# Kernel optimization log

Hardware: AMD Instinct MI355X
Metric: run time of the kernel (lower is better)

Reference implementation:

```python
import jax, jax.numpy as jnp
import numpy as np

# Production-scale dims: CSA layer on a 64x64, 512-channel decoder feature map
B, C, H, W = 8, 512, 64, 64
HOLE = 32  # centered square hole side -> M = 1024 masked points, N = 3072 context points
EPS = 1e-8


def _mask_and_indices():
    m = np.zeros((H, W), np.float32)
    r0, c0 = (H - HOLE) // 2, (W - HOLE) // 2
    m[r0:r0 + HOLE, c0:c0 + HOLE] = 1.0
    flat = m.reshape(-1)
    mask_idx = np.nonzero(flat > 0.5)[0].astype(np.int32)      # masked (hole) flat positions, raster order
    nonmask_idx = np.nonzero(flat <= 0.5)[0].astype(np.int32)  # known (context) flat positions
    return m, nonmask_idx, mask_idx


def setup_inputs() -> dict:
    key = jax.random.key(0)
    x = jax.random.normal(key, (B, C, H, W), dtype=jnp.float32)
    m, nm, mi = _mask_and_indices()
    return {
        "input": x,
        "mask": jnp.asarray(m),
        "nonmask_point_idx": jnp.asarray(nm),
        "mask_point_idx": jnp.asarray(mi),
    }


def _csa(x, nonmask_point_idx, mask_point_idx):
    """Coherent Semantic Attention with 1x1 patches (shift_sz=1, stride=1).

    For each masked location (raster order): find the most-similar context
    patch by cosine similarity, then coherently blend it with the previously
    generated patch, weighted by their respective similarities.
    """
    b, c, h, w = x.shape
    feats = x.reshape(b, c, h * w)                      # [B,C,HW] 1x1 patches
    ctx = feats[:, :, nonmask_point_idx]                # [B,C,N] known/context patches
    msk = feats[:, :, mask_point_idx]                   # [B,C,M] masked patches
    ctx_n = ctx / (jnp.linalg.norm(ctx, axis=1, keepdims=True) + EPS)
    msk_n = msk / (jnp.linalg.norm(msk, axis=1, keepdims=True) + EPS)

    # cross cosine similarity: dominant compute (B*M*N*C)
    cos = jnp.einsum('bcm,bcn->bmn', msk_n, ctx_n)      # [B,M,N]
    maxc = cos.max(axis=-1)                             # [B,M] best context similarity
    amax = cos.argmax(axis=-1)                          # [B,M]
    # gather the best-matching (unnormalized) context patch per masked point
    best = jnp.take_along_axis(ctx.transpose(0, 2, 1), amax[..., None], axis=1)  # [B,M,C]

    xs = (msk_n.transpose(2, 0, 1),   # [M,B,C] normalized masked patches
          best.transpose(1, 0, 2),    # [M,B,C] best context patches
          maxc.T)                     # [M,B]

    def step(prev, inp):
        mn, bst, mx = inp
        prev_n = prev / (jnp.linalg.norm(prev, axis=-1, keepdims=True) + EPS)
        d_ad = jnp.maximum(jnp.sum(mn * prev_n, axis=-1), 0.0)   # [B] coherence with previous generated patch
        cur = (d_ad[:, None] * prev + mx[:, None] * bst) / (d_ad + mx + EPS)[:, None]
        return cur, cur

    # prev initialized to zeros -> d_ad = 0 for the first masked patch (pure context copy)
    _, gen = jax.lax.scan(step, jnp.zeros((b, c), x.dtype), xs)   # [M,B,C]

    out = feats.at[:, :, mask_point_idx].set(gen.transpose(1, 2, 0))
    return out.reshape(b, c, h, w)


def reference(input, mask, nonmask_point_idx, mask_point_idx):
    return _csa(input, nonmask_point_idx, mask_point_idx)
```

## Files before the change

kernel.cpp:

```cpp
#include <hip/hip_runtime.h>
#include <hip/hip_bf16.h>

#define B_   8
#define C_   512
#define HW_  4096
#define M_   1024
#define N_   3072
#define EPS_ 1e-8f

typedef __attribute__((ext_vector_type(4))) float f32x4;
typedef __attribute__((ext_vector_type(8))) short short8;

__global__ void k_norms(const float* __restrict__ x, float* __restrict__ inv_all) {
    int blk = blockIdx.x;
    int b = blk >> 5;
    int chunk = blk & 31;
    int hw = chunk * 128 + threadIdx.x;
    const float* xb = x + (size_t)b * C_ * HW_;
    float acc = 0.f;
#pragma unroll 8
    for (int c = 0; c < C_; ++c) {
        float v = xb[(size_t)c * HW_ + hw];
        acc = fmaf(v, v, acc);
    }
    inv_all[b * HW_ + hw] = 1.0f / (sqrtf(acc) + EPS_);
}

__global__ __launch_bounds__(256) void k_pack(const float* __restrict__ x,
    const int* __restrict__ nm_idx, const int* __restrict__ m_idx,
    const float* __restrict__ inv_all,
    unsigned int* __restrict__ Apk, unsigned int* __restrict__ Bpk,
    float* __restrict__ invM, float* __restrict__ invC)
{
    __shared__ float T[32][513];
    __shared__ int ps[32];
    int blk = blockIdx.x;
    int t = threadIdx.x;
    int isA = blk < 256;
    int b, grp;
    const int* idxarr;
    if (isA) { b = blk >> 5; grp = blk & 31; idxarr = m_idx; }
    else     { int r = blk - 256; b = r / 96; grp = r % 96; idxarr = nm_idx; }
    const float* xb = x + (size_t)b * C_ * HW_;
    if (t < 32) {
        int p = idxarr[grp * 32 + t];
        ps[t] = p;
        float iv = inv_all[b * HW_ + p];
        if (isA) invM[b * 1024 + grp * 32 + t] = iv;
        else     invC[b * 3072 + grp * 32 + t] = iv;
    }
    __syncthreads();
#pragma unroll 4
    for (int rep = 0; rep < 64; ++rep) {
        int idx = rep * 256 + t;
        int c = idx >> 5, i = idx & 31;
        T[i][c] = xb[(size_t)c * HW_ + ps[i]];
    }
    __syncthreads();
    unsigned int* dst = isA ? (Apk + ((size_t)b * 1024 + grp * 32) * 512)
                            : (Bpk + ((size_t)b * 3072 + grp * 32) * 512);
#pragma unroll 4
    for (int rep = 0; rep < 64; ++rep) {
        int idx = rep * 256 + t;
        int i = idx >> 9, c = idx & 511;
        float v = T[i][c];
        __hip_bfloat16 h = __float2bfloat16(v);
        float hf = __bfloat162float(h);
        __hip_bfloat16 l = __float2bfloat16(v - hf);
        unsigned int hi = __bfloat16_as_ushort(h);
        unsigned int lo = __bfloat16_as_ushort(l);
        dst[(size_t)i * 512 + c] = (lo << 16) | hi;
    }
}

__global__ __launch_bounds__(256, 2) void k_cosm(
    const unsigned int* __restrict__ Apk, const unsigned int* __restrict__ Bpk,
    const float* __restrict__ invM, const float* __restrict__ invC,
    float* __restrict__ pmax, int* __restrict__ pidx)
{
    __shared__ unsigned int As[128 * 36];
    __shared__ unsigned int Bs[128 * 36];
    __shared__ float sInvM[128];
    __shared__ float sInvC[128];

    int blk = blockIdx.x;
    int b  = blk / 192;
    int r  = blk % 192;
    int mt = r / 24;
    int nt = r % 24;
    int m0 = mt * 128, n0 = nt * 128;
    int t = threadIdx.x;
    int w = t >> 6, lane = t & 63;
    int wm = (w & 1) * 64, wn = (w >> 1) * 64;
    int quad = lane >> 4, nl = lane & 15;

    if (t < 128) sInvM[t] = invM[b * 1024 + m0 + t];
    else         sInvC[t - 128] = invC[b * 3072 + n0 + (t - 128)];

    const unsigned int* gA = Apk + ((size_t)b * 1024 + m0) * 512;
    const unsigned int* gB = Bpk + ((size_t)b * 3072 + n0) * 512;

    f32x4 acc[4][4];
#pragma unroll
    for (int i = 0; i < 4; ++i)
#pragma unroll
        for (int j = 0; j < 4; ++j) acc[i][j] = (f32x4){0.f, 0.f, 0.f, 0.f};

    for (int kt = 0; kt < 16; ++kt) {
        int k0 = kt * 32;
        __syncthreads();
#pragma unroll
        for (int rep = 0; rep < 4; ++rep) {
            int idx = rep * 1024 + t * 4;
            int row = idx >> 5, col = idx & 31;
            uint4 va = *(const uint4*)(gA + (size_t)row * 512 + k0 + col);
            uint4 vb = *(const uint4*)(gB + (size_t)row * 512 + k0 + col);
            *(uint4*)&As[row * 36 + col] = va;
            *(uint4*)&Bs[row * 36 + col] = vb;
        }
        __syncthreads();

        short8 ah[4], al[4], bh[4], bl[4];
#pragma unroll
        for (int mt2 = 0; mt2 < 4; ++mt2) {
            int m = wm + mt2 * 16 + nl;
            uint4 q0 = *(const uint4*)&As[m * 36 + quad * 8];
            uint4 q1 = *(const uint4*)&As[m * 36 + quad * 8 + 4];
            uint4 H, L;
            H.x = __builtin_amdgcn_perm(q0.y, q0.x, 0x05040100u);
            H.y = __builtin_amdgcn_perm(q0.w, q0.z, 0x05040100u);
            H.z = __builtin_amdgcn_perm(q1.y, q1.x, 0x05040100u);
            H.w = __builtin_amdgcn_perm(q1.w, q1.z, 0x05040100u);
            L.x = __builtin_amdgcn_perm(q0.y, q0.x, 0x07060302u);
            L.y = __builtin_amdgcn_perm(q0.w, q0.z, 0x07060302u);
            L.z = __builtin_amdgcn_perm(q1.y, q1.x, 0x07060302u);
            L.w = __builtin_amdgcn_perm(q1.w, q1.z, 0x07060302u);
            ah[mt2] = *(short8*)&H; al[mt2] = *(short8*)&L;
        }
#pragma unroll
        for (int nt2 = 0; nt2 < 4; ++nt2) {
            int n = wn + nt2 * 16 + nl;
            uint4 q0 = *(const uint4*)&Bs[n * 36 + quad * 8];
            uint4 q1 = *(const uint4*)&Bs[n * 36 + quad * 8 + 4];
            uint4 H, L;
            H.x = __builtin_amdgcn_perm(q0.y, q0.x, 0x05040100u);
            H.y = __builtin_amdgcn_perm(q0.w, q0.z, 0x05040100u);
            H.z = __builtin_amdgcn_perm(q1.y, q1.x, 0x05040100u);
            H.w = __builtin_amdgcn_perm(q1.w, q1.z, 0x05040100u);
            L.x = __builtin_amdgcn_perm(q0.y, q0.x, 0x07060302u);
            L.y = __builtin_amdgcn_perm(q0.w, q0.z, 0x07060302u);
            L.z = __builtin_amdgcn_perm(q1.y, q1.x, 0x07060302u);
            L.w = __builtin_amdgcn_perm(q1.w, q1.z, 0x07060302u);
            bh[nt2] = *(short8*)&H; bl[nt2] = *(short8*)&L;
        }
#pragma unroll
        for (int mt2 = 0; mt2 < 4; ++mt2)
#pragma unroll
            for (int nt2 = 0; nt2 < 4; ++nt2) {
                acc[mt2][nt2] = __builtin_amdgcn_mfma_f32_16x16x32_bf16(
                    ah[mt2], bh[nt2], acc[mt2][nt2], 0, 0, 0);
                acc[mt2][nt2] = __builtin_amdgcn_mfma_f32_16x16x32_bf16(
                    ah[mt2], bl[nt2], acc[mt2][nt2], 0, 0, 0);
                acc[mt2][nt2] = __builtin_amdgcn_mfma_f32_16x16x32_bf16(
                    al[mt2], bh[nt2], acc[mt2][nt2], 0, 0, 0);
            }
    }

#pragma unroll
    for (int mt2 = 0; mt2 < 4; ++mt2)
#pragma unroll
        for (int reg = 0; reg < 4; ++reg) {
            int ml = wm + mt2 * 16 + quad * 4 + reg;
            float im = sInvM[ml];
            float v1 = -3.402823466e38f, v2 = -3.402823466e38f;
            int i1 = 0x7fffffff, i2 = 0x7fffffff;
#pragma unroll
            for (int nt2 = 0; nt2 < 4; ++nt2) {
                int nlc = wn + nt2 * 16 + nl;
                float v = acc[mt2][nt2][reg] * im * sInvC[nlc];
                int n = n0 + nlc;
                if (v > v1 || (v == v1 && n < i1)) { v2 = v1; i2 = i1; v1 = v; i1 = n; }
                else if (v > v2 || (v == v2 && n < i2)) { v2 = v; i2 = n; }
            }
#pragma unroll
            for (int off = 1; off < 16; off <<= 1) {
                float o1v = __shfl_xor(v1, off, 64); int o1i = __shfl_xor(i1, off, 64);
                float o2v = __shfl_xor(v2, off, 64); int o2i = __shfl_xor(i2, off, 64);
                if (o1v > v1 || (o1v == v1 && o1i < i1)) { v2 = v1; i2 = i1; v1 = o1v; i1 = o1i; }
                else if (o1v > v2 || (o1v == v2 && o1i < i2)) { v2 = o1v; i2 = o1i; }
                if (o2v > v1 || (o2v == v1 && o2i < i1)) { v2 = v1; i2 = i1; v1 = o2v; i1 = o2i; }
                else if (o2v > v2 || (o2v == v2 && o2i < i2)) { v2 = o2v; i2 = o2i; }
            }
            if (nl == 0) {
                int m_glob = (b << 10) + m0 + ml;
                int slot = nt * 2 + (w >> 1);
                int o = (m_glob * 48 + slot) * 2;
                pmax[o + 0] = v1; pidx[o + 0] = i1;
                pmax[o + 1] = v2; pidx[o + 1] = i2;
            }
        }
}

__global__ void k_combine(const float* __restrict__ x,
    const int* __restrict__ nm_idx, const int* __restrict__ m_idx,
    const float* __restrict__ pmax, const int* __restrict__ pidx,
    float* __restrict__ maxc, int* __restrict__ bestp)
{
    int id = blockIdx.x * 256 + threadIdx.x;
    int b = id >> 10, m = id & 1023;
    float v1 = -3.402823466e38f, v2 = -3.402823466e38f;
    int i1 = 0x7fffffff, i2 = 0x7fffffff;
#pragma unroll 8
    for (int r = 0; r < 96; ++r) {
        float v = pmax[(size_t)id * 96 + r];
        int   n = pidx[(size_t)id * 96 + r];
        if (v > v1 || (v == v1 && n < i1)) { v2 = v1; i2 = i1; v1 = v; i1 = n; }
        else if (v > v2 || (v == v2 && n < i2)) { v2 = v; i2 = n; }
    }
    if (v1 - v2 < 1e-4f) {
        const float* xb = x + (size_t)b * C_ * HW_;
        int pm = m_idx[m], p1 = nm_idx[i1], p2 = nm_idx[i2];
        double smm = 0, s11 = 0, s22 = 0, sm1 = 0, sm2 = 0;
        for (int c = 0; c < C_; ++c) {
            double xm = xb[(size_t)c * HW_ + pm];
            double xa = xb[(size_t)c * HW_ + p1];
            double xc = xb[(size_t)c * HW_ + p2];
            smm += xm * xm; s11 += xa * xa; s22 += xc * xc;
            sm1 += xm * xa; sm2 += xm * xc;
        }
        double inv_m = 1.0 / (sqrt(smm) + 1e-8);
        double c1 = sm1 * inv_m / (sqrt(s11) + 1e-8);
        double c2 = sm2 * inv_m / (sqrt(s22) + 1e-8);
        if (c2 > c1 || (c2 == c1 && i2 < i1)) { v1 = v2; i1 = i2; }
    }
    maxc[id]  = v1;
    bestp[id] = nm_idx[i1];
}

__global__ void k_copy(const float4* __restrict__ in, float4* __restrict__ out) {
    int idx = blockIdx.x * 256 + threadIdx.x;
    int stride = gridDim.x * 256;
    for (int i = idx; i < (B_ * C_ * HW_ / 4); i += stride) out[i] = in[i];
}

__global__ __launch_bounds__(256) void k_gather(const float* __restrict__ x,
    const int* __restrict__ m_idx, const float* __restrict__ inv_all,
    const int* __restrict__ bestp, float* __restrict__ mskn, float* __restrict__ best)
{
    __shared__ float T[32][513];
    __shared__ int ps[32]; __shared__ float invm[32]; __shared__ int bp[32];
    int blk = blockIdx.x;
    int b = blk >> 5, row = blk & 31;
    int m0 = row * 32;
    int t = threadIdx.x;
    const float* xb = x + (size_t)b * C_ * HW_;
    if (t < 32) {
        int p = m_idx[m0 + t];
        ps[t] = p; invm[t] = inv_all[b * HW_ + p];
        bp[t] = bestp[(b << 10) + m0 + t];
    }
    __syncthreads();
#pragma unroll 4
    for (int rep = 0; rep < 64; ++rep) {
        int idx = rep * 256 + t;
        int c = idx >> 5, i = idx & 31;
        T[i][c] = xb[(size_t)c * HW_ + ps[i]];
    }
    __syncthreads();
#pragma unroll 4
    for (int rep = 0; rep < 64; ++rep) {
        int idx = rep * 256 + t;
        int i = idx >> 9, c = idx & 511;
        mskn[((size_t)(b << 10) + m0 + i) * C_ + c] = T[i][c] * invm[i];
    }
    for (int mi = 0; mi < 32; ++mi) {
        int p = bp[mi];
        size_t o = ((size_t)(b << 10) + m0 + mi) * C_;
        for (int c = t; c < C_; c += 256)
            best[o + c] = xb[(size_t)c * HW_ + p];
    }
}

__device__ __forceinline__ float wave_sum64(float x) {
    x += __int_as_float(__builtin_amdgcn_update_dpp(0, __float_as_int(x), 0x111, 0xf, 0xf, false));
    x += __int_as_float(__builtin_amdgcn_update_dpp(0, __float_as_int(x), 0x112, 0xf, 0xf, false));
    x += __int_as_float(__builtin_amdgcn_update_dpp(0, __float_as_int(x), 0x114, 0xf, 0xf, false));
    x += __int_as_float(__builtin_amdgcn_update_dpp(0, __float_as_int(x), 0x118, 0xf, 0xf, false));
    x += __int_as_float(__builtin_amdgcn_update_dpp(0, __float_as_int(x), 0x142, 0xa, 0xf, false));
    x += __int_as_float(__builtin_amdgcn_update_dpp(0, __float_as_int(x), 0x143, 0xc, 0xf, false));
    return __int_as_float(__builtin_amdgcn_readlane(__float_as_int(x), 63));
}

__global__ __launch_bounds__(64, 1) void k_scan(const float* __restrict__ mskn,
    const float* __restrict__ best, const float* __restrict__ maxc,
    const int* __restrict__ m_idx, float* __restrict__ out)
{
    __shared__ float G[2][16 * 512];
    int b = blockIdx.x;
    int lane = threadIdx.x;
    const float4* mn4 = (const float4*)(mskn + (size_t)b * M_ * C_);
    const float4* bs4 = (const float4*)(best + (size_t)b * M_ * C_);
    const float* mx_p = maxc + b * M_;
    float* outb = out + (size_t)b * C_ * HW_;

    float pr[8];
#pragma unroll
    for (int j = 0; j < 8; ++j) pr[j] = 0.f;

    float4 mf[8][2], bf[8][2]; float mx[8];
#pragma unroll
    for (int s = 0; s < 7; ++s) {
        int base = s * 128 + lane * 2;
        mf[s][0] = mn4[base]; mf[s][1] = mn4[base + 1];
        bf[s][0] = bs4[base]; bf[s][1] = bs4[base + 1];
        mx[s] = mx_p[s];
    }

    int frow = lane >> 2;
    int fchk = lane & 3;

    int colg_prev = 0;
    for (int mb = 0; mb < 64; ++mb) {
        int p = mb & 1;
        const float* Gf = &G[p ^ 1][0];
        int colg = m_idx[mb * 16];
#pragma unroll
        for (int mi = 0; mi < 16; ++mi) {
            int m = mb * 16 + mi;
            int cur = mi & 7;
            int nxt = (mi + 7) & 7;
            if (m + 7 < M_) {
                int base = (m + 7) * 128 + lane * 2;
                mf[nxt][0] = mn4[base]; mf[nxt][1] = mn4[base + 1];
                bf[nxt][0] = bs4[base]; bf[nxt][1] = bs4[base + 1];
                mx[nxt] = mx_p[m + 7];
            }
            float4 f0, f1;
            if (mb > 0) {
                int c0 = (mi * 2) * 16 + frow;
                int c1 = (mi * 2 + 1) * 16 + frow;
                f0.x = Gf[(fchk * 4 + 0) * 512 + c0];
                f0.y = Gf[(fchk * 4 + 1) * 512 + c0];
                f0.z = Gf[(fchk * 4 + 2) * 512 + c0];
                f0.w = Gf[(fchk * 4 + 3) * 512 + c0];
                f1.x = Gf[(fchk * 4 + 0) * 512 + c1];
                f1.y = Gf[(fchk * 4 + 1) * 512 + c1];
                f1.z = Gf[(fchk * 4 + 2) * 512 + c1];
                f1.w = Gf[(fchk * 4 + 3) * 512 + c1];
            }
            __builtin_amdgcn_sched_barrier(0);
            float mn[8] = {mf[cur][0].x, mf[cur][0].y, mf[cur][0].z, mf[cur][0].w,
                           mf[cur][1].x, mf[cur][1].y, mf[cur][1].z, mf[cur][1].w};
            float bs[8] = {bf[cur][0].x, bf[cur][0].y, bf[cur][0].z, bf[cur][0].w,
                           bf[cur][1].x, bf[cur][1].y, bf[cur][1].z, bf[cur][1].w};
            float s1a = 0.f, s1b = 0.f, s2a = 0.f, s2b = 0.f;
#pragma unroll
            for (int j = 0; j < 4; ++j) {
                s1a = fmaf(pr[j], pr[j], s1a);
                s1b = fmaf(pr[j + 4], pr[j + 4], s1b);
                s2a = fmaf(mn[j], pr[j], s2a);
                s2b = fmaf(mn[j + 4], pr[j + 4], s2b);
            }
            float s1 = wave_sum64(s1a + s1b);
            float s2 = wave_sum64(s2a + s2b);
            float mxc = mx[cur];
            float d_ad = fmaxf(s2, 0.f) * __builtin_amdgcn_rcpf(sqrtf(s1) + EPS_);
            float inv  = __builtin_amdgcn_rcpf(d_ad + mxc + EPS_);
#pragma unroll
            for (int j = 0; j < 8; ++j)
                pr[j] = (d_ad * pr[j] + mxc * bs[j]) * inv;
            float4 o0 = {pr[0], pr[1], pr[2], pr[3]};
            float4 o1 = {pr[4], pr[5], pr[6], pr[7]};
            *(float4*)&G[p][mi * 512 + lane * 8]     = o0;
            *(float4*)&G[p][mi * 512 + lane * 8 + 4] = o1;
            if (mb > 0) {
                int c0 = (mi * 2) * 16 + frow;
                int c1 = (mi * 2 + 1) * 16 + frow;
                *(float4*)&outb[(size_t)c0 * HW_ + colg_prev + fchk * 4] = f0;
                *(float4*)&outb[(size_t)c1 * HW_ + colg_prev + fchk * 4] = f1;
            }
        }
        colg_prev = colg;
    }
    const float* Gf = &G[1][0];
#pragma unroll 4
    for (int r = 0; r < 32; ++r) {
        int c = r * 16 + frow;
        float4 v;
        v.x = Gf[(fchk * 4 + 0) * 512 + c];
        v.y = Gf[(fchk * 4 + 1) * 512 + c];
        v.z = Gf[(fchk * 4 + 2) * 512 + c];
        v.w = Gf[(fchk * 4 + 3) * 512 + c];
        *(float4*)&outb[(size_t)c * HW_ + colg_prev + fchk * 4] = v;
    }
}

extern "C" void kernel_launch(void* const* d_in, const int* in_sizes, int n_in,
                              void* d_out, int out_size, void* d_ws, size_t ws_size,
                              hipStream_t stream) {
    (void)in_sizes; (void)n_in; (void)out_size; (void)ws_size;
    const float* x      = (const float*)d_in[0];
    const int*   nm_idx = (const int*)d_in[2];
    const int*   m_idx  = (const int*)d_in[3];
    float* out = (float*)d_out;
    char* ws = (char*)d_ws;

    float* inv_all = (float*)(ws + 0);
    float* invM    = (float*)(ws + 131072);
    float* invC    = (float*)(ws + 163840);
    float* pmax    = (float*)(ws + 262144);
    int*   pidx    = (int*)  (ws + 3407872);
    float* maxc    = (float*)(ws + 6553600);
    int*   bestp   = (int*)  (ws + 6586368);
    unsigned int* Apk = (unsigned int*)(ws + 6619136);
    unsigned int* Bpk = (unsigned int*)(ws + 23396352);
    float* mskn = (float*)Apk;
    float* best = (float*)Bpk;

    hipLaunchKernelGGL(k_norms,   dim3(256),  dim3(128), 0, stream, x, inv_all);
    hipLaunchKernelGGL(k_pack,    dim3(1024), dim3(256), 0, stream, x, nm_idx, m_idx, inv_all, Apk, Bpk, invM, invC);
    hipLaunchKernelGGL(k_cosm,    dim3(1536), dim3(256), 0, stream, Apk, Bpk, invM, invC, pmax, pidx);
    hipLaunchKernelGGL(k_combine, dim3(32),   dim3(256), 0, stream, x, nm_idx, m_idx, pmax, pidx, maxc, bestp);
    hipLaunchKernelGGL(k_copy,    dim3(2048), dim3(256), 0, stream, (const float4*)x, (float4*)out);
    hipLaunchKernelGGL(k_gather,  dim3(256),  dim3(256), 0, stream, x, m_idx, inv_all, bestp, mskn, best);
    hipLaunchKernelGGL(k_scan,    dim3(8),    dim3(64),  0, stream, mskn, best, maxc, m_idx, out);
}
```

Baseline: 853.4 us.

## Split scan output: write contiguous gen buffer, scatter-transpose in separate kernel

```diff
diff --git a/kernel.cpp b/kernel.cpp
--- a/kernel.cpp
+++ b/kernel.cpp
@@ -293,15 +293,14 @@
 
 __global__ __launch_bounds__(64, 1) void k_scan(const float* __restrict__ mskn,
     const float* __restrict__ best, const float* __restrict__ maxc,
-    const int* __restrict__ m_idx, float* __restrict__ out)
-{
-    __shared__ float G[2][16 * 512];
+    float* __restrict__ gen)
+{
     int b = blockIdx.x;
     int lane = threadIdx.x;
     const float4* mn4 = (const float4*)(mskn + (size_t)b * M_ * C_);
     const float4* bs4 = (const float4*)(best + (size_t)b * M_ * C_);
     const float* mx_p = maxc + b * M_;
-    float* outb = out + (size_t)b * C_ * HW_;
+    float4* gen4 = (float4*)(gen + (size_t)b * M_ * C_);
 
     float pr[8];
 #pragma unroll
@@ -316,18 +315,11 @@
         mx[s] = mx_p[s];
     }
 
-    int frow = lane >> 2;
-    int fchk = lane & 3;
-
-    int colg_prev = 0;
-    for (int mb = 0; mb < 64; ++mb) {
-        int p = mb & 1;
-        const float* Gf = &G[p ^ 1][0];
-        int colg = m_idx[mb * 16];
-#pragma unroll
-        for (int mi = 0; mi < 16; ++mi) {
-            int m = mb * 16 + mi;
-            int cur = mi & 7;
+    for (int mb = 0; mb < 128; ++mb) {
+#pragma unroll
+        for (int mi = 0; mi < 8; ++mi) {
+            int m = mb * 8 + mi;
+            int cur = mi;
             int nxt = (mi + 7) & 7;
             if (m + 7 < M_) {
                 int base = (m + 7) * 128 + lane * 2;
@@ -335,20 +327,6 @@
                 bf[nxt][0] = bs4[base]; bf[nxt][1] = bs4[base + 1];
                 mx[nxt] = mx_p[m + 7];
             }
-            float4 f0, f1;
-            if (mb > 0) {
-                int c0 = (mi * 2) * 16 + frow;
-                int c1 = (mi * 2 + 1) * 16 + frow;
-                f0.x = Gf[(fchk * 4 + 0) * 512 + c0];
-                f0.y = Gf[(fchk * 4 + 1) * 512 + c0];
-                f0.z = Gf[(fchk * 4 + 2) * 512 + c0];
-                f0.w = Gf[(fchk * 4 + 3) * 512 + c0];
-                f1.x = Gf[(fchk * 4 + 0) * 512 + c1];
-                f1.y = Gf[(fchk * 4 + 1) * 512 + c1];
-                f1.z = Gf[(fchk * 4 + 2) * 512 + c1];
-                f1.w = Gf[(fchk * 4 + 3) * 512 + c1];
-            }
-            __builtin_amdgcn_sched_barrier(0);
             float mn[8] = {mf[cur][0].x, mf[cur][0].y, mf[cur][0].z, mf[cur][0].w,
                            mf[cur][1].x, mf[cur][1].y, mf[cur][1].z, mf[cur][1].w};
             float bs[8] = {bf[cur][0].x, bf[cur][0].y, bf[cur][0].z, bf[cur][0].w,
@@ -371,27 +349,34 @@
                 pr[j] = (d_ad * pr[j] + mxc * bs[j]) * inv;
             float4 o0 = {pr[0], pr[1], pr[2], pr[3]};
             float4 o1 = {pr[4], pr[5], pr[6], pr[7]};
-            *(float4*)&G[p][mi * 512 + lane * 8]     = o0;
-            *(float4*)&G[p][mi * 512 + lane * 8 + 4] = o1;
-            if (mb > 0) {
-                int c0 = (mi * 2) * 16 + frow;
-                int c1 = (mi * 2 + 1) * 16 + frow;
-                *(float4*)&outb[(size_t)c0 * HW_ + colg_prev + fchk * 4] = f0;
-                *(float4*)&outb[(size_t)c1 * HW_ + colg_prev + fchk * 4] = f1;
-            }
-        }
-        colg_prev = colg;
-    }
-    const float* Gf = &G[1][0];
-#pragma unroll 4
-    for (int r = 0; r < 32; ++r) {
-        int c = r * 16 + frow;
-        float4 v;
-        v.x = Gf[(fchk * 4 + 0) * 512 + c];
-        v.y = Gf[(fchk * 4 + 1) * 512 + c];
-        v.z = Gf[(fchk * 4 + 2) * 512 + c];
-        v.w = Gf[(fchk * 4 + 3) * 512 + c];
-        *(float4*)&outb[(size_t)c * HW_ + colg_prev + fchk * 4] = v;
+            gen4[m * 128 + lane * 2]     = o0;
+            gen4[m * 128 + lane * 2 + 1] = o1;
+        }
+    }
+}
+
+__global__ __launch_bounds__(256) void k_scatter(const float* __restrict__ gen,
+    const int* __restrict__ m_idx, float* __restrict__ out)
+{
+    __shared__ float T[32][513];
+    int blk = blockIdx.x;
+    int b = blk >> 5, row = blk & 31;
+    int m0 = row * 32;
+    int t = threadIdx.x;
+#pragma unroll 4
+    for (int rep = 0; rep < 64; ++rep) {
+        int idx = rep * 256 + t;
+        int i = idx >> 9, c = idx & 511;
+        T[i][c] = gen[((size_t)(b << 10) + m0 + i) * C_ + c];
+    }
+    __syncthreads();
+    int colg = m_idx[m0];
+    float* outb = out + (size_t)b * C_ * HW_;
+#pragma unroll 4
+    for (int rep = 0; rep < 64; ++rep) {
+        int idx = rep * 256 + t;
+        int c = idx >> 5, i = idx & 31;
+        outb[(size_t)c * HW_ + colg + i] = T[i][c];
     }
 }
 
@@ -416,6 +401,7 @@
     unsigned int* Bpk = (unsigned int*)(ws + 23396352);
     float* mskn = (float*)Apk;
     float* best = (float*)Bpk;
+    float* gen  = (float*)(ws + 23396352 + 16777216);
 
     hipLaunchKernelGGL(k_norms,   dim3(256),  dim3(128), 0, stream, x, inv_all);
     hipLaunchKernelGGL(k_pack,    dim3(1024), dim3(256), 0, stream, x, nm_idx, m_idx, inv_all, Apk, Bpk, invM, invC);
@@ -423,5 +409,6 @@
     hipLaunchKernelGGL(k_combine, dim3(32),   dim3(256), 0, stream, x, nm_idx, m_idx, pmax, pidx, maxc, bestp);
     hipLaunchKernelGGL(k_copy,    dim3(2048), dim3(256), 0, stream, (const float4*)x, (float4*)out);
     hipLaunchKernelGGL(k_gather,  dim3(256),  dim3(256), 0, stream, x, m_idx, inv_all, bestp, mskn, best);
-    hipLaunchKernelGGL(k_scan,    dim3(8),    dim3(64),  0, stream, mskn, best, maxc, m_idx, out);
-}
+    hipLaunchKernelGGL(k_scan,    dim3(8),    dim3(64),  0, stream, mskn, best, maxc, gen);
+    hipLaunchKernelGGL(k_scatter, dim3(256),  dim3(256), 0, stream, gen, m_idx, out);
+}
```

Result: faster. 733.0 us (-14.1%).
